# Kernel optimization log

Measured on AMD Instinct MI355X. Metric: run time of the kernel, lower is better.

## Reference

```python
import jax, jax.numpy as jnp
import numpy as np

B, H, I, E = 16, 16, 512, 512  # batch, heads, input_dim, embedding_dim (I must == E for matmul(q,k))


def setup_inputs() -> dict:
    key = jax.random.key(0)
    k_x, k_q, k_k, k_v, k_w, k_b = jax.random.split(key, 6)
    return {
        "x": jax.random.normal(k_x, (B, 1, I, E), dtype=jnp.float32),
        "W_q": jax.random.normal(k_q, (1, H, I, E), dtype=jnp.float32),
        "W_k": jax.random.normal(k_k, (1, H, I, E), dtype=jnp.float32),
        "W_v": jax.random.normal(k_v, (1, H, I, E), dtype=jnp.float32),
        "mlp_w": jax.random.normal(k_w, (E, E), dtype=jnp.float32) * (1.0 / np.sqrt(E)),
        "mlp_b": jnp.zeros((E,), dtype=jnp.float32),
    }


def reference(x, W_q, W_k, W_v, mlp_w, mlp_b):
    # Broadcast elementwise "projections": [B,1,I,E] * [1,H,I,E] -> [B,H,I,E]
    q = x * W_q
    k = x * W_k
    v = x * W_v
    scale = jnp.sqrt(jnp.asarray(E, dtype=x.dtype))
    # matmul with NO transpose of keys (as in the original): [B,H,I,E]@[B,H,I,E] needs E==I
    scores = jnp.matmul(q, k) / scale            # [B,H,I,I]
    attn = jax.nn.softmax(scores, axis=2)        # softmax over dim=2 (rows), faithful to source
    emb = jnp.sum(jnp.matmul(attn, v), axis=2)   # [B,H,I,E] summed over I -> [B,H,E]
    return emb @ mlp_w.T + mlp_b                 # nn.Linear: x @ W^T + b -> [B,H,E]
```

## Files before the change

kernel.cpp:

```cpp
#include <hip/hip_runtime.h>
#include <hip/hip_bf16.h>

#define B_ 16
#define H_ 16
#define I_ 512
#define E_ 512


#define NSLICE 8

__global__ __launch_bounds__(256) void k_emb_part(const float* __restrict__ x,
                                                  const float* __restrict__ Wv,
                                                  float2* __restrict__ part) {
    const int E2 = E_ / 2;
    const int e2_0  = blockIdx.x * 64;
    const int b0    = blockIdx.y * 4;
    const int h0    = (blockIdx.z & 3) * 4;
    const int slice = blockIdx.z >> 2;
    const int lane  = threadIdx.x & 63;
    const int wave  = threadIdx.x >> 6;

    const float2* x2 = (const float2*)x;
    const float2* w2 = (const float2*)Wv;

    float2 acc[4][4];
#pragma unroll
    for (int bi = 0; bi < 4; ++bi)
#pragma unroll
        for (int hj = 0; hj < 4; ++hj) { acc[bi][hj].x = 0.f; acc[bi][hj].y = 0.f; }

    const float2* xp[4];
    const float2* wp[4];
#pragma unroll
    for (int bi = 0; bi < 4; ++bi) xp[bi] = x2 + (size_t)(b0 + bi) * I_ * E2 + e2_0 + lane;
#pragma unroll
    for (int hj = 0; hj < 4; ++hj) wp[hj] = w2 + (size_t)(h0 + hj) * I_ * E2 + e2_0 + lane;

    const int ib = slice * 64 + wave * 16;
    for (int ii = 0; ii < 16; ++ii) {
        const int off = (ib + ii) * E2;
        float2 xv[4], wv[4];
#pragma unroll
        for (int bi = 0; bi < 4; ++bi) xv[bi] = xp[bi][off];
#pragma unroll
        for (int hj = 0; hj < 4; ++hj) wv[hj] = wp[hj][off];
#pragma unroll
        for (int bi = 0; bi < 4; ++bi)
#pragma unroll
            for (int hj = 0; hj < 4; ++hj) {
                acc[bi][hj].x = fmaf(xv[bi].x, wv[hj].x, acc[bi][hj].x);
                acc[bi][hj].y = fmaf(xv[bi].y, wv[hj].y, acc[bi][hj].y);
            }
    }

    __shared__ float2 red[4][16][64];
#pragma unroll
    for (int bi = 0; bi < 4; ++bi)
#pragma unroll
        for (int hj = 0; hj < 4; ++hj)
            red[wave][bi * 4 + hj][lane] = acc[bi][hj];
    __syncthreads();

    for (int t = threadIdx.x; t < 16 * 64; t += 256) {
        const int pair = t >> 6, le = t & 63;
        float2 s0 = red[0][pair][le], s1 = red[1][pair][le];
        float2 s2 = red[2][pair][le], s3 = red[3][pair][le];
        float2 s; s.x = (s0.x + s1.x) + (s2.x + s3.x); s.y = (s0.y + s1.y) + (s2.y + s3.y);
        const int row = (b0 + (pair >> 2)) * H_ + h0 + (pair & 3);
        part[((size_t)slice * (B_ * H_) + row) * E2 + e2_0 + le] = s;
    }
}

__global__ __launch_bounds__(256) void k_reduce(const float4* __restrict__ part,
                                                float4* __restrict__ emb) {
    const int idx = blockIdx.x * 256 + threadIdx.x;
    const int sl_stride = (B_ * H_ * E_) / 4;
    float4 s = part[idx];
#pragma unroll
    for (int sl = 1; sl < NSLICE; ++sl) {
        float4 p = part[sl * sl_stride + idx];
        s.x += p.x; s.y += p.y; s.z += p.z; s.w += p.w;
    }
    emb[idx] = s;
}

#define MT 16
#define NT 32
#define KT 64

__global__ __launch_bounds__(256) void k_mlp(const float* __restrict__ emb,
                                             const float* __restrict__ W,
                                             const float* __restrict__ bias,
                                             float* __restrict__ out) {
    const int cblk = blockIdx.x;
    const int rblk = blockIdx.y;

    __shared__ float As[KT][MT + 1];
    __shared__ float Ws[KT][NT + 1];

    const int tx = threadIdx.x & 15;
    const int ty = threadIdx.x >> 4;

    float acc0 = 0.f, acc1 = 0.f;

    const int alr = threadIdx.x >> 4;
    const int alk = (threadIdx.x & 15) * 4;
    const int wlr = threadIdx.x >> 3;
    const int wlk = (threadIdx.x & 7) * 8;

    for (int k0 = 0; k0 < E_; k0 += KT) {
        float4 a = *(const float4*)(emb + (size_t)(rblk * MT + alr) * E_ + k0 + alk);
        As[alk + 0][alr] = a.x; As[alk + 1][alr] = a.y;
        As[alk + 2][alr] = a.z; As[alk + 3][alr] = a.w;

        const float* wsrc = W + (size_t)(cblk * NT + wlr) * E_ + k0 + wlk;
        float4 w0 = *(const float4*)wsrc;
        float4 w1 = *(const float4*)(wsrc + 4);
        Ws[wlk + 0][wlr] = w0.x; Ws[wlk + 1][wlr] = w0.y;
        Ws[wlk + 2][wlr] = w0.z; Ws[wlk + 3][wlr] = w0.w;
        Ws[wlk + 4][wlr] = w1.x; Ws[wlk + 5][wlr] = w1.y;
        Ws[wlk + 6][wlr] = w1.z; Ws[wlk + 7][wlr] = w1.w;
        __syncthreads();

#pragma unroll
        for (int k = 0; k < KT; ++k) {
            const float a0 = As[k][ty];
            const float w0 = Ws[k][tx * 2 + 0];
            const float w1 = Ws[k][tx * 2 + 1];
            acc0 = fmaf(a0, w0, acc0);
            acc1 = fmaf(a0, w1, acc1);
        }
        __syncthreads();
    }

    const int r = rblk * MT + ty;
    const int c = cblk * NT + tx * 2;
    out[(size_t)r * E_ + c + 0] = acc0 + bias[c + 0];
    out[(size_t)r * E_ + c + 1] = acc1 + bias[c + 1];
}

extern "C" void kernel_launch(void* const* d_in, const int* in_sizes, int n_in,
                              void* d_out, int out_size, void* d_ws, size_t ws_size,
                              hipStream_t stream) {
    const float* x     = (const float*)d_in[0];
    const float* W_v   = (const float*)d_in[3];
    const float* mlp_w = (const float*)d_in[4];
    const float* mlp_b = (const float*)d_in[5];
    float* out = (float*)d_out;

    float* part = (float*)d_ws;
    float* emb  = part + (size_t)NSLICE * B_ * H_ * E_;

    dim3 g1(E_ / 128, B_ / 4, (H_ / 4) * NSLICE);
    k_emb_part<<<g1, 256, 0, stream>>>(x, W_v, (float2*)part);

    k_reduce<<<(B_ * H_ * E_ / 4) / 256, 256, 0, stream>>>((const float4*)part,
                                                           (float4*)emb);

    dim3 g3(E_ / NT, (B_ * H_) / MT);
    k_mlp<<<g3, 256, 0, stream>>>(emb, mlp_w, mlp_b, out);
}
```

Baseline: 123.3 us.

## Enlarge emb register tile to 8x8, split-K the MLP with separate bias reduce

The emb partial kernel now gives each thread an 8x8 batch-by-head accumulator tile of scalars instead of 4x4 float2, and doubles the I-slices to 16. This raises reuse of each loaded x and W_v element and cuts global traffic per FMA. The MLP GEMM is split over K into 8 partial blocks, each using a 4x4 register tile with float4 shared loads, followed by a reduce kernel that adds the bias. The cost is more partial-sum traffic, an extra launch, and higher register pressure from the 64 accumulators.

```diff
diff --git a/kernel.cpp b/kernel.cpp
--- a/kernel.cpp
+++ b/kernel.cpp
@@ -7,136 +7,163 @@
 #define E_ 512
 
 
-#define NSLICE 8
+#define NSLICE 16
+#define KSPLIT 8
 
 __global__ __launch_bounds__(256) void k_emb_part(const float* __restrict__ x,
                                                   const float* __restrict__ Wv,
-                                                  float2* __restrict__ part) {
-    const int E2 = E_ / 2;
-    const int e2_0  = blockIdx.x * 64;
-    const int b0    = blockIdx.y * 4;
-    const int h0    = (blockIdx.z & 3) * 4;
-    const int slice = blockIdx.z >> 2;
+                                                  float* __restrict__ part) {
+    const int e     = blockIdx.x * 64 + (threadIdx.x & 63);
+    const int b0    = blockIdx.y * 8;
+    const int h0    = (blockIdx.z & 1) * 8;
+    const int slice = blockIdx.z >> 1;
     const int lane  = threadIdx.x & 63;
     const int wave  = threadIdx.x >> 6;
 
-    const float2* x2 = (const float2*)x;
-    const float2* w2 = (const float2*)Wv;
+    float acc[8][8];
+#pragma unroll
+    for (int bi = 0; bi < 8; ++bi)
+#pragma unroll
+        for (int hj = 0; hj < 8; ++hj) acc[bi][hj] = 0.0f;
 
-    float2 acc[4][4];
+    const int ibase = slice * 32 + wave * 8;
+    const float* xp[8];
+    const float* wp[8];
 #pragma unroll
-    for (int bi = 0; bi < 4; ++bi)
+    for (int bi = 0; bi < 8; ++bi)
+        xp[bi] = x + ((size_t)(b0 + bi) * I_ + ibase) * E_ + e;
 #pragma unroll
-        for (int hj = 0; hj < 4; ++hj) { acc[bi][hj].x = 0.f; acc[bi][hj].y = 0.f; }
+    for (int hj = 0; hj < 8; ++hj)
+        wp[hj] = Wv + ((size_t)(h0 + hj) * I_ + ibase) * E_ + e;
 
-    const float2* xp[4];
-    const float2* wp[4];
+    for (int ii = 0; ii < 8; ++ii) {
+        const int off = ii * E_;
+        float xv[8], wv[8];
 #pragma unroll
-    for (int bi = 0; bi < 4; ++bi) xp[bi] = x2 + (size_t)(b0 + bi) * I_ * E2 + e2_0 + lane;
+        for (int bi = 0; bi < 8; ++bi) xv[bi] = xp[bi][off];
 #pragma unroll
-    for (int hj = 0; hj < 4; ++hj) wp[hj] = w2 + (size_t)(h0 + hj) * I_ * E2 + e2_0 + lane;
-
-    const int ib = slice * 64 + wave * 16;
-    for (int ii = 0; ii < 16; ++ii) {
-        const int off = (ib + ii) * E2;
-        float2 xv[4], wv[4];
+        for (int hj = 0; hj < 8; ++hj) wv[hj] = wp[hj][off];
 #pragma unroll
-        for (int bi = 0; bi < 4; ++bi) xv[bi] = xp[bi][off];
+        for (int bi = 0; bi < 8; ++bi)
 #pragma unroll
-        for (int hj = 0; hj < 4; ++hj) wv[hj] = wp[hj][off];
-#pragma unroll
-        for (int bi = 0; bi < 4; ++bi)
-#pragma unroll
-            for (int hj = 0; hj < 4; ++hj) {
-                acc[bi][hj].x = fmaf(xv[bi].x, wv[hj].x, acc[bi][hj].x);
-                acc[bi][hj].y = fmaf(xv[bi].y, wv[hj].y, acc[bi][hj].y);
-            }
+            for (int hj = 0; hj < 8; ++hj)
+                acc[bi][hj] = fmaf(xv[bi], wv[hj], acc[bi][hj]);
     }
 
-    __shared__ float2 red[4][16][64];
+    __shared__ float red[4][64][64];
 #pragma unroll
-    for (int bi = 0; bi < 4; ++bi)
+    for (int bi = 0; bi < 8; ++bi)
 #pragma unroll
-        for (int hj = 0; hj < 4; ++hj)
-            red[wave][bi * 4 + hj][lane] = acc[bi][hj];
+        for (int hj = 0; hj < 8; ++hj)
+            red[wave][bi * 8 + hj][lane] = acc[bi][hj];
     __syncthreads();
 
-    for (int t = threadIdx.x; t < 16 * 64; t += 256) {
+    for (int t = threadIdx.x; t < 64 * 64; t += 256) {
         const int pair = t >> 6, le = t & 63;
-        float2 s0 = red[0][pair][le], s1 = red[1][pair][le];
-        float2 s2 = red[2][pair][le], s3 = red[3][pair][le];
-        float2 s; s.x = (s0.x + s1.x) + (s2.x + s3.x); s.y = (s0.y + s1.y) + (s2.y + s3.y);
-        const int row = (b0 + (pair >> 2)) * H_ + h0 + (pair & 3);
-        part[((size_t)slice * (B_ * H_) + row) * E2 + e2_0 + le] = s;
+        float s = (red[0][pair][le] + red[1][pair][le]) +
+                  (red[2][pair][le] + red[3][pair][le]);
+        const int row = (b0 + (pair >> 3)) * H_ + h0 + (pair & 7);
+        part[((size_t)slice * (B_ * H_) + row) * E_ + blockIdx.x * 64 + le] = s;
     }
 }
 
-__global__ __launch_bounds__(256) void k_reduce(const float4* __restrict__ part,
-                                                float4* __restrict__ emb) {
+__global__ __launch_bounds__(256) void k_emb_reduce(const float4* __restrict__ part,
+                                                    float4* __restrict__ emb) {
     const int idx = blockIdx.x * 256 + threadIdx.x;
-    const int sl_stride = (B_ * H_ * E_) / 4;
+    const int sl  = (B_ * H_ * E_) / 4;
     float4 s = part[idx];
 #pragma unroll
-    for (int sl = 1; sl < NSLICE; ++sl) {
-        float4 p = part[sl * sl_stride + idx];
+    for (int j = 1; j < NSLICE; ++j) {
+        float4 p = part[(size_t)j * sl + idx];
         s.x += p.x; s.y += p.y; s.z += p.z; s.w += p.w;
     }
     emb[idx] = s;
 }
 
-#define MT 16
-#define NT 32
-#define KT 64
-
-__global__ __launch_bounds__(256) void k_mlp(const float* __restrict__ emb,
-                                             const float* __restrict__ W,
-                                             const float* __restrict__ bias,
-                                             float* __restrict__ out) {
+__global__ __launch_bounds__(128) void k_mlp_part(const float* __restrict__ emb,
+                                                  const float* __restrict__ W,
+                                                  float* __restrict__ part) {
     const int cblk = blockIdx.x;
     const int rblk = blockIdx.y;
+    const int k0   = blockIdx.z * 64;
 
-    __shared__ float As[KT][MT + 1];
-    __shared__ float Ws[KT][NT + 1];
+    __shared__ float As[32][68];
+    __shared__ float Ws[64][68];
 
-    const int tx = threadIdx.x & 15;
-    const int ty = threadIdx.x >> 4;
+    const int t = threadIdx.x;
 
-    float acc0 = 0.f, acc1 = 0.f;
+    {
+        const int r8 = t >> 4, kq = t & 15;
+#pragma unroll
+        for (int it = 0; it < 4; ++it) {
+            const int r = r8 + it * 8;
+            float4 v = *(const float4*)(emb + (size_t)(rblk * 32 + r) * E_ + k0 + kq * 4);
+            *(float4*)&As[r][kq * 4] = v;
+        }
+    }
+    {
+        const int c8 = t >> 4, kq = t & 15;
+#pragma unroll
+        for (int it = 0; it < 8; ++it) {
+            const int c = c8 + it * 8;
+            float4 v = *(const float4*)(W + (size_t)(cblk * 64 + c) * E_ + k0 + kq * 4);
+            Ws[kq * 4 + 0][c] = v.x;
+            Ws[kq * 4 + 1][c] = v.y;
+            Ws[kq * 4 + 2][c] = v.z;
+            Ws[kq * 4 + 3][c] = v.w;
+        }
+    }
+    __syncthreads();
 
-    const int alr = threadIdx.x >> 4;
-    const int alk = (threadIdx.x & 15) * 4;
-    const int wlr = threadIdx.x >> 3;
-    const int wlk = (threadIdx.x & 7) * 8;
+    const int tx = t & 15, ty = t >> 4;
+    const int c0 = tx * 4, r0 = ty * 4;
 
-    for (int k0 = 0; k0 < E_; k0 += KT) {
-        float4 a = *(const float4*)(emb + (size_t)(rblk * MT + alr) * E_ + k0 + alk);
-        As[alk + 0][alr] = a.x; As[alk + 1][alr] = a.y;
-        As[alk + 2][alr] = a.z; As[alk + 3][alr] = a.w;
+    float4 acc0 = {0, 0, 0, 0}, acc1 = {0, 0, 0, 0};
+    float4 acc2 = {0, 0, 0, 0}, acc3 = {0, 0, 0, 0};
 
-        const float* wsrc = W + (size_t)(cblk * NT + wlr) * E_ + k0 + wlk;
-        float4 w0 = *(const float4*)wsrc;
-        float4 w1 = *(const float4*)(wsrc + 4);
-        Ws[wlk + 0][wlr] = w0.x; Ws[wlk + 1][wlr] = w0.y;
-        Ws[wlk + 2][wlr] = w0.z; Ws[wlk + 3][wlr] = w0.w;
-        Ws[wlk + 4][wlr] = w1.x; Ws[wlk + 5][wlr] = w1.y;
-        Ws[wlk + 6][wlr] = w1.z; Ws[wlk + 7][wlr] = w1.w;
-        __syncthreads();
-
-#pragma unroll
-        for (int k = 0; k < KT; ++k) {
-            const float a0 = As[k][ty];
-            const float w0 = Ws[k][tx * 2 + 0];
-            const float w1 = Ws[k][tx * 2 + 1];
-            acc0 = fmaf(a0, w0, acc0);
-            acc1 = fmaf(a0, w1, acc1);
-        }
-        __syncthreads();
+    for (int k = 0; k < 64; k += 4) {
+        float4 a0 = *(const float4*)&As[r0 + 0][k];
+        float4 a1 = *(const float4*)&As[r0 + 1][k];
+        float4 a2 = *(const float4*)&As[r0 + 2][k];
+        float4 a3 = *(const float4*)&As[r0 + 3][k];
+        float4 w0 = *(const float4*)&Ws[k + 0][c0];
+        float4 w1 = *(const float4*)&Ws[k + 1][c0];
+        float4 w2 = *(const float4*)&Ws[k + 2][c0];
+        float4 w3 = *(const float4*)&Ws[k + 3][c0];
+#define MLP_STEP(ACC, AV)                                                  \
+        ACC.x = fmaf(AV.x, w0.x, fmaf(AV.y, w1.x, fmaf(AV.z, w2.x, fmaf(AV.w, w3.x, ACC.x)))); \
+        ACC.y = fmaf(AV.x, w0.y, fmaf(AV.y, w1.y, fmaf(AV.z, w2.y, fmaf(AV.w, w3.y, ACC.y)))); \
+        ACC.z = fmaf(AV.x, w0.z, fmaf(AV.y, w1.z, fmaf(AV.z, w2.z, fmaf(AV.w, w3.z, ACC.z)))); \
+        ACC.w = fmaf(AV.x, w0.w, fmaf(AV.y, w1.w, fmaf(AV.z, w2.w, fmaf(AV.w, w3.w, ACC.w))));
+        MLP_STEP(acc0, a0)
+        MLP_STEP(acc1, a1)
+        MLP_STEP(acc2, a2)
+        MLP_STEP(acc3, a3)
+#undef MLP_STEP
     }
 
-    const int r = rblk * MT + ty;
-    const int c = cblk * NT + tx * 2;
-    out[(size_t)r * E_ + c + 0] = acc0 + bias[c + 0];
-    out[(size_t)r * E_ + c + 1] = acc1 + bias[c + 1];
+    float* dst = part + ((size_t)blockIdx.z * (B_ * H_) + rblk * 32 + r0) * E_ +
+                 cblk * 64 + c0;
+    *(float4*)(dst + 0 * E_) = acc0;
+    *(float4*)(dst + 1 * E_) = acc1;
+    *(float4*)(dst + 2 * E_) = acc2;
+    *(float4*)(dst + 3 * E_) = acc3;
+}
+
+__global__ __launch_bounds__(256) void k_out(const float4* __restrict__ part,
+                                             const float4* __restrict__ bias,
+                                             float4* __restrict__ out) {
+    const int idx = blockIdx.x * 256 + threadIdx.x;
+    const int sl  = (B_ * H_ * E_) / 4;
+    float4 s = part[idx];
+#pragma unroll
+    for (int j = 1; j < KSPLIT; ++j) {
+        float4 p = part[(size_t)j * sl + idx];
+        s.x += p.x; s.y += p.y; s.z += p.z; s.w += p.w;
+    }
+    float4 bv = bias[idx & (E_ / 4 - 1)];
+    s.x += bv.x; s.y += bv.y; s.z += bv.z; s.w += bv.w;
+    out[idx] = s;
 }
 
 extern "C" void kernel_launch(void* const* d_in, const int* in_sizes, int n_in,
@@ -148,15 +175,19 @@
     const float* mlp_b = (const float*)d_in[5];
     float* out = (float*)d_out;
 
-    float* part = (float*)d_ws;
-    float* emb  = part + (size_t)NSLICE * B_ * H_ * E_;
+    float* epart = (float*)d_ws;
+    float* emb   = epart + (size_t)NSLICE * B_ * H_ * E_;
+    float* mpart = emb + (size_t)B_ * H_ * E_;
 
-    dim3 g1(E_ / 128, B_ / 4, (H_ / 4) * NSLICE);
-    k_emb_part<<<g1, 256, 0, stream>>>(x, W_v, (float2*)part);
+    dim3 g1(E_ / 64, B_ / 8, (H_ / 8) * NSLICE);
+    k_emb_part<<<g1, 256, 0, stream>>>(x, W_v, epart);
 
-    k_reduce<<<(B_ * H_ * E_ / 4) / 256, 256, 0, stream>>>((const float4*)part,
-                                                           (float4*)emb);
+    k_emb_reduce<<<(B_ * H_ * E_ / 4) / 256, 256, 0, stream>>>(
+        (const float4*)epart, (float4*)emb);
 
-    dim3 g3(E_ / NT, (B_ * H_) / MT);
-    k_mlp<<<g3, 256, 0, stream>>>(emb, mlp_w, mlp_b, out);
+    dim3 g3(E_ / 64, (B_ * H_) / 32, KSPLIT);
+    k_mlp_part<<<g3, 128, 0, stream>>>(emb, mlp_w, mpart);
+
+    k_out<<<(B_ * H_ * E_ / 4) / 256, 256, 0, stream>>>(
+        (const float4*)mpart, (const float4*)mlp_b, (float4*)out);
 }
```

Result: faster. 112.8 us (-8.5%).
